# Performance work log

Measured on AMD Instinct MI355X. Metric: run time of the kernel, lower is better.

Reference implementation:

```python
import jax, jax.numpy as jnp
import numpy as np

N = 400000      # simplices (edges of the complexes)
E = 2400000     # nnz of each Laplacian
F_IN = 32
H = 64
KAPPA = 3
G = 512         # graphs in batch
N_OUT = 8
EPS = 1e-5


def spmm(edge_index, edge_values, x, n):
    # y[i] = sum_e val_e * x[j],  i = edge_index[0], j = edge_index[1]
    msg = edge_values[:, None] * x[edge_index[1]]
    return jax.ops.segment_sum(msg, edge_index[0], num_segments=n)


def sc_layer(x, li, lv, ui, uv, Wl, bl, Wu, bu, Wh, bh):
    # SCNN layer: z_low + z_up + z_har (aggr_x fused in)
    n = x.shape[0]
    z = x @ Wh + bh                       # harmonic / identity term
    xl = x
    for k in range(KAPPA):
        xl = spmm(li, lv, xl, n)          # L_low^{k+1} x
        z = z + xl @ Wl[k] + bl[k]
    xu = x
    for k in range(KAPPA):
        xu = spmm(ui, uv, xu, n)          # L_up^{k+1} x
        z = z + xu @ Wu[k] + bu[k]
    return z


def batch_norm(x, gamma, beta):
    mean = jnp.mean(x, axis=0)
    var = jnp.mean((x - mean) ** 2, axis=0)   # biased, as torch BN training
    return (x - mean) * jax.lax.rsqrt(var + EPS) * gamma + beta


def setup_inputs() -> dict:
    key = jax.random.key(0)
    ks = jax.random.split(key, 32)
    s_in = 1.0 / np.sqrt(F_IN)
    s_h = 1.0 / np.sqrt(H)
    inp = {
        "x": jax.random.normal(ks[0], (N, F_IN), jnp.float32),
        "lower_edge_index": jax.random.randint(ks[1], (2, E), 0, N),
        "lower_edge_values": jax.random.normal(ks[2], (E,), jnp.float32),
        "upper_edge_index": jax.random.randint(ks[3], (2, E), 0, N),
        "upper_edge_values": jax.random.normal(ks[4], (E,), jnp.float32),
        "batch_index": jnp.sort(jax.random.randint(ks[5], (N,), 0, G)),
        # layer 0 (F_IN -> H)
        "l0_Wl": jax.random.normal(ks[6], (KAPPA, F_IN, H), jnp.float32) * s_in,
        "l0_bl": jnp.zeros((KAPPA, H), jnp.float32),
        "l0_Wu": jax.random.normal(ks[7], (KAPPA, F_IN, H), jnp.float32) * s_in,
        "l0_bu": jnp.zeros((KAPPA, H), jnp.float32),
        "l0_Wh": jax.random.normal(ks[8], (F_IN, H), jnp.float32) * s_in,
        "l0_bh": jnp.zeros((H,), jnp.float32),
        # layer 1 (H -> H)
        "l1_Wl": jax.random.normal(ks[9], (KAPPA, H, H), jnp.float32) * s_h,
        "l1_bl": jnp.zeros((KAPPA, H), jnp.float32),
        "l1_Wu": jax.random.normal(ks[10], (KAPPA, H, H), jnp.float32) * s_h,
        "l1_bu": jnp.zeros((KAPPA, H), jnp.float32),
        "l1_Wh": jax.random.normal(ks[11], (H, H), jnp.float32) * s_h,
        "l1_bh": jnp.zeros((H,), jnp.float32),
        # batch norms
        "bn0_g": jnp.ones((H,), jnp.float32),
        "bn0_b": jnp.zeros((H,), jnp.float32),
        "bn1_g": jnp.ones((H,), jnp.float32),
        "bn1_b": jnp.zeros((H,), jnp.float32),
        # output MLP [2H, H, N_OUT]
        "mlp_W1": jax.random.normal(ks[12], (2 * H, H), jnp.float32) / np.sqrt(2 * H),
        "mlp_b1": jnp.zeros((H,), jnp.float32),
        "mlp_W2": jax.random.normal(ks[13], (H, N_OUT), jnp.float32) * s_h,
        "mlp_b2": jnp.zeros((N_OUT,), jnp.float32),
    }
    return inp


def reference(x, lower_edge_values, upper_edge_values,
              l0_Wl, l0_bl, l0_Wu, l0_bu, l0_Wh, l0_bh,
              l1_Wl, l1_bl, l1_Wu, l1_bu, l1_Wh, l1_bh,
              bn0_g, bn0_b, bn1_g, bn1_b,
              mlp_W1, mlp_b1, mlp_W2, mlp_b2,
              lower_edge_index, upper_edge_index, batch_index):
    li, ui, bi = lower_edge_index, upper_edge_index, batch_index
    lv, uv = lower_edge_values, upper_edge_values

    h = sc_layer(x, li, lv, ui, uv, l0_Wl, l0_bl, l0_Wu, l0_bu, l0_Wh, l0_bh)
    h = jax.nn.elu(batch_norm(h, bn0_g, bn0_b))
    h = sc_layer(h, li, lv, ui, uv, l1_Wl, l1_bl, l1_Wu, l1_bu, l1_Wh, l1_bh)
    h = jax.nn.elu(batch_norm(h, bn1_g, bn1_b))

    # global max pool + global mean pool per graph
    gmax = jax.ops.segment_max(h, bi, num_segments=G)
    gsum = jax.ops.segment_sum(h, bi, num_segments=G)
    cnt = jax.ops.segment_sum(jnp.ones((h.shape[0],), h.dtype), bi, num_segments=G)
    gmean = gsum / jnp.maximum(cnt, 1.0)[:, None]
    g = jax.nn.elu(jnp.concatenate([gmax, gmean], axis=1))  # [G, 2H]

    # MLP [2H -> H -> N_OUT]
    g = jax.nn.relu(g @ mlp_W1 + mlp_b1)
    return g @ mlp_W2 + mlp_b2
```

## Files before the change

### kernel.cpp

```cpp
#include <hip/hip_runtime.h>
#include <hip/hip_bf16.h>
#include <math.h>

#define N_SIMP 400000
#define E_NNZ  2400000
#define FIN    32
#define HDIM   64
#define KAPPA  3
#define G_NUM  512
#define NOUT   8
#define BN_EPS 1e-5

#define NDIG_HALF 391
#define NDIG      782
#define P1_EDGES  16384
#define P1_BLOCKS 293
#define P1_T      1024
#define P1_EPT    16
#define P2_CAP    7168
#define P2_T      512
#define P2_ITERS  14

typedef __hip_bfloat16 bf16;
typedef _Float16 f16;
typedef short s8v __attribute__((ext_vector_type(8)));
typedef ushort u8v __attribute__((ext_vector_type(8)));
typedef _Float16 h8v __attribute__((ext_vector_type(8)));
typedef float f4v __attribute__((ext_vector_type(4)));

__device__ __forceinline__ float elu_f(float x) {
    return x > 0.f ? x : expm1f(x);
}
__device__ __forceinline__ float bf2f(ushort u) {
    return __uint_as_float(((unsigned int)u) << 16);
}
__device__ __forceinline__ ushort f2bf(float f) {
    bf16 h = (bf16)f;
    return *(ushort*)&h;
}


__global__ __launch_bounds__(P1_T, 1) void p1_sort_kernel(
        const int* __restrict__ eiL, const float* __restrict__ lv,
        const int* __restrict__ eiU, const float* __restrict__ uv,
        int* __restrict__ ccnt, int* __restrict__ bofsv,
        int2* __restrict__ coarse) {
    __shared__ int2 rec[P1_EDGES];
    __shared__ int h[NDIG];
    __shared__ int hscan[P1_T];
    int t = threadIdx.x;
    for (int j = t; j < NDIG; j += P1_T) h[j] = 0;
    __syncthreads();
    int base_i = blockIdx.x * P1_EDGES;
    int key[P1_EPT], val[P1_EPT], dg[P1_EPT];
#pragma unroll
    for (int k = 0; k < P1_EPT; ++k) {
        int i = base_i + k * P1_T + t;
        int dd = -1;
        if (i < 2 * E_NNZ) {
            int row, col;
            float v;
            if (i < E_NNZ) {
                row = eiL[i]; col = eiL[E_NNZ + i]; v = lv[i];
                dd = row >> 10;
            } else {
                int e = i - E_NNZ;
                row = eiU[e]; col = eiU[E_NNZ + e]; v = uv[e];
                dd = NDIG_HALF + (row >> 10);
            }
            key[k] = ((row & 1023) << 22) | col;
            val[k] = __float_as_int(v);
            atomicAdd(&h[dd], 1);
        }
        dg[k] = dd;
    }
    __syncthreads();
    int cv = (t < NDIG) ? h[t] : 0;
    hscan[t] = cv;
    __syncthreads();
    for (int off = 1; off < P1_T; off <<= 1) {
        int x = (t >= off) ? hscan[t - off] : 0;
        __syncthreads();
        hscan[t] += x;
        __syncthreads();
    }
    if (t < NDIG) {
        int ex = hscan[t] - cv;
        ccnt[blockIdx.x * NDIG + t] = cv;
        bofsv[blockIdx.x * NDIG + t] = ex;
        h[t] = ex;
    }
    __syncthreads();
#pragma unroll
    for (int k = 0; k < P1_EPT; ++k) {
        if (dg[k] >= 0) {
            int pos = atomicAdd(&h[dg[k]], 1);
            rec[pos] = make_int2(key[k], val[k]);
        }
    }
    __syncthreads();
    int2* dst = coarse + (size_t)blockIdx.x * P1_EDGES;
    int nrec = 2 * E_NNZ - base_i;
    if (nrec > P1_EDGES) nrec = P1_EDGES;
    for (int j = t; j < nrec; j += P1_T) dst[j] = rec[j];
}

__global__ void digit_total_kernel(const int* __restrict__ cnt, int* __restrict__ tot) {
    int d = blockIdx.x * 256 + threadIdx.x;
    if (d >= NDIG) return;
    int run = 0;
    for (int b = 0; b < P1_BLOCKS; ++b) run += cnt[b * NDIG + d];
    tot[d] = run;
}

__global__ __launch_bounds__(1024) void scan_base_kernel(int* __restrict__ tot) {
    __shared__ int s[1024];
    int t = threadIdx.x;
    int v = (t < NDIG) ? tot[t] : 0;
    s[t] = v;
    __syncthreads();
    for (int off = 1; off < 1024; off <<= 1) {
        int x = (t >= off) ? s[t - off] : 0;
        __syncthreads();
        s[t] += x;
        __syncthreads();
    }
    if (t < NDIG) tot[t] = s[t] - v;
    if (t == 1023) tot[NDIG] = s[1023];
}


__global__ __launch_bounds__(P2_T) void p2_build_kernel(
        const int2* __restrict__ coarse, const int* __restrict__ ccnt,
        const int* __restrict__ bofsv, const int* __restrict__ basev,
        int* __restrict__ rpL, int* __restrict__ rpU,
        int2* __restrict__ edgeL, int2* __restrict__ edgeU) {
    __shared__ int pk[P2_CAP];
    __shared__ int vl[P2_CAP];
    __shared__ int hist[1024];
    __shared__ int sc[P2_T];
    __shared__ int fo[P1_BLOCKS];
    __shared__ int stot;
    int d = blockIdx.x;
    int t = threadIdx.x;
    int len = 0, ofs = 0;
    if (t < P1_BLOCKS) { len = ccnt[t * NDIG + d]; ofs = bofsv[t * NDIG + d]; }
    sc[t] = len;
    __syncthreads();
    for (int off = 1; off < P2_T; off <<= 1) {
        int x = (t >= off) ? sc[t - off] : 0;
        __syncthreads();
        sc[t] += x;
        __syncthreads();
    }
    if (t < P1_BLOCKS) { fo[t] = sc[t] - len; hist[t] = len; hist[512 + t] = ofs; }
    if (t == P1_BLOCKS - 1) stot = sc[t];
    __syncthreads();
    int sz = stot;
    if (sz > P2_CAP) sz = P2_CAP;
    int wv = t >> 6, lane = t & 63;
    for (int b = wv; b < P1_BLOCKS; b += P2_T / 64) {
        int L = hist[b], O = hist[512 + b], F = fo[b];
        const int2* sp = coarse + (size_t)b * P1_EDGES + O;
        for (int j = lane; j < L; j += 64) {
            int dst2 = F + j;
            if (dst2 < P2_CAP) {
                int2 r = sp[j];
                pk[dst2] = r.x;
                vl[dst2] = r.y;
            }
        }
    }
    __syncthreads();
    hist[t] = 0;
    hist[t + P2_T] = 0;
    __syncthreads();
    int myrank[P2_ITERS];
#pragma unroll
    for (int k = 0; k < P2_ITERS; ++k) {
        int j = k * P2_T + t;
        myrank[k] = (j < sz) ? atomicAdd(&hist[((unsigned)pk[j]) >> 22], 1) : 0;
    }
    __syncthreads();
    int h0 = hist[2 * t], h1 = hist[2 * t + 1];
    sc[t] = h0 + h1;
    __syncthreads();
    for (int off = 1; off < P2_T; off <<= 1) {
        int x = (t >= off) ? sc[t - off] : 0;
        __syncthreads();
        sc[t] += x;
        __syncthreads();
    }
    int pbase = sc[t] - (h0 + h1);
    __syncthreads();
    hist[2 * t] = pbase;
    hist[2 * t + 1] = pbase + h0;
    int which = (d >= NDIG_HALF);
    int lbase = basev[d] - (which ? E_NNZ : 0);
    int rowbase = (which ? d - NDIG_HALF : d) << 10;
    int* rp = which ? rpU : rpL;
    int r0 = rowbase + 2 * t, r1 = r0 + 1;
    if (r0 < N_SIMP) rp[r0] = lbase + pbase;
    if (r1 < N_SIMP) rp[r1] = lbase + pbase + h0;
    __syncthreads();
    int2* eout = which ? edgeU : edgeL;
#pragma unroll
    for (int k = 0; k < P2_ITERS; ++k) {
        int j = k * P2_T + t;
        if (j < sz) {
            unsigned p = (unsigned)pk[j];
            int pos = lbase + hist[p >> 22] + myrank[k];
            eout[pos] = make_int2((int)(p & 0x3FFFFF), vl[j]);
        }
    }
}


__global__ void combine_bias_kernel(const float* __restrict__ bh,
                                    const float* __restrict__ bl,
                                    const float* __restrict__ bu,
                                    float* __restrict__ out) {
    int h = threadIdx.x;
    float acc = bh[h];
    for (int k = 0; k < KAPPA; ++k) acc += bl[k * HDIM + h] + bu[k * HDIM + h];
    out[h] = acc;
}

__global__ void f32_to_bf16_kernel(const float* __restrict__ in, bf16* __restrict__ out) {
    int idx = blockIdx.x * 256 + threadIdx.x;
    float4 v = ((const float4*)in)[idx];
    ushort4 w;
    w.x = f2bf(v.x); w.y = f2bf(v.y); w.z = f2bf(v.z); w.w = f2bf(v.w);
    ((ushort4*)out)[idx] = w;
}

__global__ void wtrans_all_kernel(const float* __restrict__ s0, const float* __restrict__ s1,
                                  const float* __restrict__ s2, const float* __restrict__ s3,
                                  const float* __restrict__ s4, const float* __restrict__ s5,
                                  ushort* __restrict__ wt) {
    int idx = blockIdx.x * 256 + threadIdx.x;
    const float* src; int Ktot, off;
    if (idx < 2048)       { src = s0; Ktot = 32;  off = 0; }
    else if (idx < 6144)  { src = s1; Ktot = 64;  off = 2048; }
    else if (idx < 12288) { src = s2; Ktot = 96;  off = 6144; }
    else if (idx < 18432) { src = s3; Ktot = 96;  off = 12288; }
    else if (idx < 30720) { src = s4; Ktot = 192; off = 18432; }
    else                  { src = s5; Ktot = 192; off = 30720; }
    int rel = idx - off;
    int n = rel / Ktot, kk = rel - n * Ktot;
    wt[idx] = f2bf(src[kk * 64 + n]);
}


__global__ void spmm32_kernel(const int* __restrict__ rp, const int2* __restrict__ edge,
                              const bf16* __restrict__ srcb, int src_stride,
                              bf16* __restrict__ dstb) {
    const ushort* src = (const ushort*)srcb;
    ushort* dst = (ushort*)dstb;
    int tid = threadIdx.x;
    int lane = tid & 63;
    int wv = tid >> 6;
    int grp = lane >> 2;
    int li = lane & 3;
    int row = blockIdx.x * 64 + wv * 16 + grp;
    int s = rp[row];
    int e = (row == N_SIMP - 1) ? E_NNZ : rp[row + 1];
    int deg = e - s;
    float a[8] = {0.f, 0.f, 0.f, 0.f, 0.f, 0.f, 0.f, 0.f};
    if (deg > 0) {
        int2 ed[8];
#pragma unroll
        for (int t = 0; t < 8; ++t) {
            int j = s + t;
            ed[t] = edge[(j < e) ? j : (e - 1)];
        }
        u8v xs[8];
#pragma unroll
        for (int t = 0; t < 8; ++t)
            xs[t] = *(const u8v*)(src + (size_t)ed[t].x * src_stride + li * 8);
#pragma unroll
        for (int t = 0; t < 8; ++t) {
            float v = (t < deg) ? __int_as_float(ed[t].y) : 0.f;
#pragma unroll
            for (int c = 0; c < 8; ++c) a[c] += v * bf2f(xs[t][c]);
        }
        for (int j = s + 8; j < e; j += 4) {
            int2 e2[4];
#pragma unroll
            for (int t = 0; t < 4; ++t) {
                int jj = j + t;
                e2[t] = edge[(jj < e) ? jj : (e - 1)];
            }
            u8v x2[4];
#pragma unroll
            for (int t = 0; t < 4; ++t)
                x2[t] = *(const u8v*)(src + (size_t)e2[t].x * src_stride + li * 8);
#pragma unroll
            for (int t = 0; t < 4; ++t) {
                float v = (j + t < e) ? __int_as_float(e2[t].y) : 0.f;
#pragma unroll
                for (int c = 0; c < 8; ++c) a[c] += v * bf2f(x2[t][c]);
            }
        }
    }
    u8v w;
#pragma unroll
    for (int c = 0; c < 8; ++c) w[c] = f2bf(a[c]);
    *(u8v*)(dst + (size_t)row * 32 + li * 8) = w;
}

__global__ void spmm64_kernel(const int* __restrict__ rp, const int2* __restrict__ edge,
                              const bf16* __restrict__ srcb, bf16* __restrict__ dstb) {
    const ushort* src = (const ushort*)srcb;
    ushort* dst = (ushort*)dstb;
    int tid = threadIdx.x;
    int lane = tid & 63;
    int wv = tid >> 6;
    int grp = lane >> 3;
    int li = lane & 7;
    int row = blockIdx.x * 32 + wv * 8 + grp;
    int s = rp[row];
    int e = (row == N_SIMP - 1) ? E_NNZ : rp[row + 1];
    int deg = e - s;
    float a[8] = {0.f, 0.f, 0.f, 0.f, 0.f, 0.f, 0.f, 0.f};
    if (deg > 0) {
        int2 ed[8];
#pragma unroll
        for (int t = 0; t < 8; ++t) {
            int j = s + t;
            ed[t] = edge[(j < e) ? j : (e - 1)];
        }
        u8v xs[8];
#pragma unroll
        for (int t = 0; t < 8; ++t)
            xs[t] = *(const u8v*)(src + (size_t)ed[t].x * 64 + li * 8);
#pragma unroll
        for (int t = 0; t < 8; ++t) {
            float v = (t < deg) ? __int_as_float(ed[t].y) : 0.f;
#pragma unroll
            for (int c = 0; c < 8; ++c) a[c] += v * bf2f(xs[t][c]);
        }
        for (int j = s + 8; j < e; j += 4) {
            int2 e2[4];
#pragma unroll
            for (int t = 0; t < 4; ++t) {
                int jj = j + t;
                e2[t] = edge[(jj < e) ? jj : (e - 1)];
            }
            u8v x2[4];
#pragma unroll
            for (int t = 0; t < 4; ++t)
                x2[t] = *(const u8v*)(src + (size_t)e2[t].x * 64 + li * 8);
#pragma unroll
            for (int t = 0; t < 4; ++t) {
                float v = (j + t < e) ? __int_as_float(e2[t].y) : 0.f;
#pragma unroll
                for (int c = 0; c < 8; ++c) a[c] += v * bf2f(x2[t][c]);
            }
        }
    }
    u8v w;
#pragma unroll
    for (int c = 0; c < 8; ++c) w[c] = f2bf(a[c]);
    *(u8v*)(dst + (size_t)row * 64 + li * 8) = w;
}


template <int NCH, int NCH1, bool INIT>
__global__ __launch_bounds__(256) void mfma_gemm_kernel(
        const ushort* __restrict__ s0, int st0,
        const ushort* __restrict__ s1, int st1,
        const ushort* __restrict__ s2, int st2,
        const ushort* __restrict__ s3, int st3,
        const ushort* __restrict__ s4, int st4,
        const ushort* __restrict__ s5, int st5,
        const ushort* __restrict__ Wt1, int Kstride1,
        const ushort* __restrict__ Wt2, int Kstride2,
        const float* __restrict__ bias,
        f16* __restrict__ z) {
    int tid = threadIdx.x;
    int wv = tid >> 6, lane = tid & 63;
    int quad = lane >> 4, n = lane & 15;
    int rowbase = blockIdx.x * 64 + wv * 16;
    int arow = rowbase + n;

    f4v acc0 = {0.f, 0.f, 0.f, 0.f};
    f4v acc1 = {0.f, 0.f, 0.f, 0.f};
    f4v acc2 = {0.f, 0.f, 0.f, 0.f};
    f4v acc3 = {0.f, 0.f, 0.f, 0.f};

#pragma unroll
    for (int ch = 0; ch < NCH; ++ch) {
        const ushort* sp = (ch == 0) ? s0 : (ch == 1) ? s1 : (ch == 2) ? s2
                         : (ch == 3) ? s3 : (ch == 4) ? s4 : s5;
        int st = (ch == 0) ? st0 : (ch == 1) ? st1 : (ch == 2) ? st2
               : (ch == 3) ? st3 : (ch == 4) ? st4 : st5;
        const ushort* wb = (ch < NCH1) ? (Wt1 + ch * 32) : (Wt2 + (ch - NCH1) * 32);
        int Ks = (ch < NCH1) ? Kstride1 : Kstride2;
        s8v a = *(const s8v*)(sp + (size_t)arow * st + quad * 8);
        const ushort* wq = wb + quad * 8;
        s8v b0 = *(const s8v*)(wq + (size_t)(0 * 16 + n) * Ks);
        s8v b1 = *(const s8v*)(wq + (size_t)(1 * 16 + n) * Ks);
        s8v b2 = *(const s8v*)(wq + (size_t)(2 * 16 + n) * Ks);
        s8v b3 = *(const s8v*)(wq + (size_t)(3 * 16 + n) * Ks);
        acc0 = __builtin_amdgcn_mfma_f32_16x16x32_bf16(a, b0, acc0, 0, 0, 0);
        acc1 = __builtin_amdgcn_mfma_f32_16x16x32_bf16(a, b1, acc1, 0, 0, 0);
        acc2 = __builtin_amdgcn_mfma_f32_16x16x32_bf16(a, b2, acc2, 0, 0, 0);
        acc3 = __builtin_amdgcn_mfma_f32_16x16x32_bf16(a, b3, acc3, 0, 0, 0);
    }
#pragma unroll
    for (int r = 0; r < 4; ++r) {
        int orow = rowbase + quad * 4 + r;
        f16* zp = z + (size_t)orow * 64 + n;
        if (INIT) {
            zp[0]  = (f16)(bias[n]      + acc0[r]);
            zp[16] = (f16)(bias[16 + n] + acc1[r]);
            zp[32] = (f16)(bias[32 + n] + acc2[r]);
            zp[48] = (f16)(bias[48 + n] + acc3[r]);
        } else {
            zp[0]  = (f16)((float)zp[0]  + acc0[r]);
            zp[16] = (f16)((float)zp[16] + acc1[r]);
            zp[32] = (f16)((float)zp[32] + acc2[r]);
            zp[48] = (f16)((float)zp[48] + acc3[r]);
        }
    }
}


__global__ void bn_stats_kernel(const f16* __restrict__ z, double* __restrict__ stats) {
    __shared__ float ss[256 * 8], qq[256 * 8];
    int tid = threadIdx.x;
    const h8v* z8 = (const h8v*)z;
    const int total8 = N_SIMP * HDIM / 8;
    float fs[8] = {0, 0, 0, 0, 0, 0, 0, 0};
    float fq[8] = {0, 0, 0, 0, 0, 0, 0, 0};
    for (int i = blockIdx.x * 256 + tid; i < total8; i += (int)gridDim.x * 256) {
        h8v v = z8[i];
#pragma unroll
        for (int c = 0; c < 8; ++c) {
            float f = (float)v[c];
            fs[c] += f;
            fq[c] += f * f;
        }
    }
#pragma unroll
    for (int c = 0; c < 8; ++c) { ss[tid * 8 + c] = fs[c]; qq[tid * 8 + c] = fq[c]; }
    __syncthreads();
    if (tid < 64) {
        int sel = tid >> 3, slot = tid & 7;
        double a = 0.0, b = 0.0;
#pragma unroll 8
        for (int k = 0; k < 32; ++k) {
            int t = sel + (k << 3);
            a += (double)ss[t * 8 + slot];
            b += (double)qq[t * 8 + slot];
        }
        atomicAdd(&stats[tid], a);
        atomicAdd(&stats[64 + tid], b);
    }
}

__global__ void bn_elu_bf16_kernel(const f16* __restrict__ z, const double* __restrict__ stats,
                                   const float* __restrict__ gamma, const float* __restrict__ beta,
                                   bf16* __restrict__ out) {
    __shared__ float scale_s[64], shift_s[64];
    int tid = threadIdx.x;
    if (tid < 64) {
        double mean = stats[tid] / (double)N_SIMP;
        double var = stats[64 + tid] / (double)N_SIMP - mean * mean;
        double sc = (double)gamma[tid] / sqrt(var + BN_EPS);
        scale_s[tid] = (float)sc;
        shift_s[tid] = (float)((double)beta[tid] - mean * sc);
    }
    __syncthreads();
    const h8v* z8 = (const h8v*)z;
    u8v* o8 = (u8v*)out;
    const int total8 = N_SIMP * HDIM / 8;
    int hb = (tid & 7) * 8;
    for (int i = blockIdx.x * 256 + tid; i < total8; i += (int)gridDim.x * 256) {
        h8v v = z8[i];
        u8v w;
#pragma unroll
        for (int c = 0; c < 8; ++c)
            w[c] = f2bf(elu_f((float)v[c] * scale_s[hb + c] + shift_s[hb + c]));
        o8[i] = w;
    }
}

__global__ void bn_elu_f16_kernel(f16* __restrict__ z, const double* __restrict__ stats,
                                  const float* __restrict__ gamma, const float* __restrict__ beta) {
    __shared__ float scale_s[64], shift_s[64];
    int tid = threadIdx.x;
    if (tid < 64) {
        double mean = stats[tid] / (double)N_SIMP;
        double var = stats[64 + tid] / (double)N_SIMP - mean * mean;
        double sc = (double)gamma[tid] / sqrt(var + BN_EPS);
        scale_s[tid] = (float)sc;
        shift_s[tid] = (float)((double)beta[tid] - mean * sc);
    }
    __syncthreads();
    h8v* z8 = (h8v*)z;
    const int total8 = N_SIMP * HDIM / 8;
    int hb = (tid & 7) * 8;
    for (int i = blockIdx.x * 256 + tid; i < total8; i += (int)gridDim.x * 256) {
        h8v v = z8[i];
        h8v w;
#pragma unroll
        for (int c = 0; c < 8; ++c)
            w[c] = (f16)elu_f((float)v[c] * scale_s[hb + c] + shift_s[hb + c]);
        z8[i] = w;
    }
}

__global__ void pool_kernel(const f16* __restrict__ hbuf, const int* __restrict__ bidx,
                            float* __restrict__ gbuf) {
    __shared__ float smax[256], ssum[256];
    int g = blockIdx.x;
    int tid = threadIdx.x;
    int lo = 0, hi = N_SIMP;
    while (lo < hi) { int mid = (lo + hi) >> 1; if (bidx[mid] < g) lo = mid + 1; else hi = mid; }
    int start = lo;
    hi = N_SIMP;
    while (lo < hi) { int mid = (lo + hi) >> 1; if (bidx[mid] < g + 1) lo = mid + 1; else hi = mid; }
    int end = lo;
    int h = tid & 63, rep = tid >> 6;
    float mx = -INFINITY, sm = 0.f;
    for (int i = start + rep; i < end; i += 4) {
        float v = (float)hbuf[(size_t)i * HDIM + h];
        mx = fmaxf(mx, v);
        sm += v;
    }
    smax[tid] = mx; ssum[tid] = sm;
    __syncthreads();
    if (tid < 64) {
        float m = fmaxf(fmaxf(smax[tid], smax[tid + 64]), fmaxf(smax[tid + 128], smax[tid + 192]));
        float s = ssum[tid] + ssum[tid + 64] + ssum[tid + 128] + ssum[tid + 192];
        int cnt = end - start;
        float mean = s / fmaxf((float)cnt, 1.f);
        gbuf[g * 128 + tid] = elu_f(m);
        gbuf[g * 128 + 64 + tid] = elu_f(mean);
    }
}

__global__ void mlp_kernel(const float* __restrict__ gbuf, const float* __restrict__ W1,
                           const float* __restrict__ b1, const float* __restrict__ W2,
                           const float* __restrict__ b2, float* __restrict__ out) {
    __shared__ float gs[128];
    __shared__ float hs[64];
    int g = blockIdx.x, tid = threadIdx.x;
    gs[tid] = gbuf[g * 128 + tid];
    gs[64 + tid] = gbuf[g * 128 + 64 + tid];
    __syncthreads();
    float acc = b1[tid];
#pragma unroll
    for (int k = 0; k < 128; ++k) acc += gs[k] * W1[k * 64 + tid];
    hs[tid] = fmaxf(acc, 0.f);
    __syncthreads();
    if (tid < 8) {
        float o = b2[tid];
#pragma unroll
        for (int k = 0; k < 64; ++k) o += hs[k] * W2[k * 8 + tid];
        out[g * 8 + tid] = o;
    }
}


extern "C" void kernel_launch(void* const* d_in, const int* in_sizes, int n_in,
                              void* d_out, int out_size, void* d_ws, size_t ws_size,
                              hipStream_t stream) {
    const float* x     = (const float*)d_in[0];
    const int*   li    = (const int*)d_in[1];
    const float* lv    = (const float*)d_in[2];
    const int*   ui    = (const int*)d_in[3];
    const float* uv    = (const float*)d_in[4];
    const int*   bidx  = (const int*)d_in[5];
    const float* l0_Wl = (const float*)d_in[6];
    const float* l0_bl = (const float*)d_in[7];
    const float* l0_Wu = (const float*)d_in[8];
    const float* l0_bu = (const float*)d_in[9];
    const float* l0_Wh = (const float*)d_in[10];
    const float* l0_bh = (const float*)d_in[11];
    const float* l1_Wl = (const float*)d_in[12];
    const float* l1_bl = (const float*)d_in[13];
    const float* l1_Wu = (const float*)d_in[14];
    const float* l1_bu = (const float*)d_in[15];
    const float* l1_Wh = (const float*)d_in[16];
    const float* l1_bh = (const float*)d_in[17];
    const float* bn0_g = (const float*)d_in[18];
    const float* bn0_b = (const float*)d_in[19];
    const float* bn1_g = (const float*)d_in[20];
    const float* bn1_b = (const float*)d_in[21];
    const float* mW1   = (const float*)d_in[22];
    const float* mb1   = (const float*)d_in[23];
    const float* mW2   = (const float*)d_in[24];
    const float* mb2   = (const float*)d_in[25];
    float* out = (float*)d_out;

    char* base = (char*)d_ws;
    f16*   z     = (f16*)base;
    bf16*  h0bf  = (bf16*)(base + 51200000ull);
    bf16*  g1    = (bf16*)(base + 102400000ull);
    bf16*  g2    = (bf16*)(base + 153600000ull);
    int2*  edgeL = (int2*)(base + 204800000ull);
    int2*  edgeU = (int2*)(base + 224000000ull);
    int*   rpL   = (int*)(base + 243200000ull);
    int*   rpU   = (int*)(base + 244800032ull);
    double* stats = (double*)(base + 246404160ull);
    float* cbias  = (float*)(base + 246405184ull);
    float* gbuf   = (float*)(base + 246405440ull);
    ushort* wt    = (ushort*)(base + 246667584ull);

    int2* coarse = (int2*)base;
    int*  basev  = (int*)(base + 38500000ull);
    int*  ccnt   = (int*)(base + 51200000ull);
    int*  bofsv  = (int*)(base + 52200000ull);

    bf16* xbf  = g1;
    bf16* cAL  = g1 + (size_t)N_SIMP * 32;
    bf16* cBL  = g2;
    bf16* cCL  = g2 + (size_t)N_SIMP * 32;
    bf16* cAU  = h0bf;
    bf16* cBU  = h0bf + (size_t)N_SIMP * 32;
    bf16* cCU  = g1;

    ushort* wt_l0h = wt;
    ushort* wt_l1h = wt + 2048;
    ushort* wt_l0l = wt + 6144;
    ushort* wt_l0u = wt + 12288;
    ushort* wt_l1l = wt + 18432;
    ushort* wt_l1u = wt + 30720;

    const int SP32_BLOCKS = N_SIMP / 64;
    const int SP64_BLOCKS = N_SIMP / 32;
    const int MF_BLOCKS   = N_SIMP / 64;

    wtrans_all_kernel<<<168, 256, 0, stream>>>(l0_Wh, l1_Wh, l0_Wl, l0_Wu, l1_Wl, l1_Wu, wt);
    f32_to_bf16_kernel<<<N_SIMP * 32 / 4 / 256, 256, 0, stream>>>(x, xbf);

    p1_sort_kernel<<<P1_BLOCKS, P1_T, 0, stream>>>(li, lv, ui, uv, ccnt, bofsv, coarse);
    digit_total_kernel<<<(NDIG + 255) / 256, 256, 0, stream>>>(ccnt, basev);
    scan_base_kernel<<<1, 1024, 0, stream>>>(basev);
    p2_build_kernel<<<NDIG, P2_T, 0, stream>>>(coarse, ccnt, bofsv, basev,
                                               rpL, rpU, edgeL, edgeU);

    const ushort* xbfu = (const ushort*)xbf;
    const ushort* h0u  = (const ushort*)h0bf;
    const ushort* g1u  = (const ushort*)g1;
    const ushort* g2u  = (const ushort*)g2;

    combine_bias_kernel<<<1, 64, 0, stream>>>(l0_bh, l0_bl, l0_bu, cbias);
    mfma_gemm_kernel<1, 1, true><<<MF_BLOCKS, 256, 0, stream>>>(
        xbfu, 32, nullptr, 0, nullptr, 0, nullptr, 0, nullptr, 0, nullptr, 0,
        wt_l0h, 32, wt_l0h, 32, cbias, z);

    spmm32_kernel<<<SP32_BLOCKS, 256, 0, stream>>>(rpL, edgeL, xbf, 32, cAL);
    spmm32_kernel<<<SP32_BLOCKS, 256, 0, stream>>>(rpL, edgeL, cAL, 32, cBL);
    spmm32_kernel<<<SP32_BLOCKS, 256, 0, stream>>>(rpL, edgeL, cBL, 32, cCL);
    spmm32_kernel<<<SP32_BLOCKS, 256, 0, stream>>>(rpU, edgeU, xbf, 32, cAU);
    spmm32_kernel<<<SP32_BLOCKS, 256, 0, stream>>>(rpU, edgeU, cAU, 32, cBU);
    spmm32_kernel<<<SP32_BLOCKS, 256, 0, stream>>>(rpU, edgeU, cBU, 32, cCU);
    mfma_gemm_kernel<6, 3, false><<<MF_BLOCKS, 256, 0, stream>>>(
        (const ushort*)cAL, 32, (const ushort*)cBL, 32, (const ushort*)cCL, 32,
        (const ushort*)cAU, 32, (const ushort*)cBU, 32, (const ushort*)cCU, 32,
        wt_l0l, 96, wt_l0u, 96, nullptr, z);

    (void)hipMemsetAsync(stats, 0, 128 * sizeof(double), stream);
    bn_stats_kernel<<<1024, 256, 0, stream>>>(z, stats);
    bn_elu_bf16_kernel<<<1024, 256, 0, stream>>>(z, stats, bn0_g, bn0_b, h0bf);

    combine_bias_kernel<<<1, 64, 0, stream>>>(l1_bh, l1_bl, l1_bu, cbias);
    mfma_gemm_kernel<2, 2, true><<<MF_BLOCKS, 256, 0, stream>>>(
        h0u, 64, h0u + 32, 64, nullptr, 0, nullptr, 0, nullptr, 0, nullptr, 0,
        wt_l1h, 64, wt_l1h, 64, cbias, z);

    spmm64_kernel<<<SP64_BLOCKS, 256, 0, stream>>>(rpL, edgeL, h0bf, g1);
    spmm64_kernel<<<SP64_BLOCKS, 256, 0, stream>>>(rpL, edgeL, g1, g2);
    mfma_gemm_kernel<4, 4, false><<<MF_BLOCKS, 256, 0, stream>>>(
        g1u, 64, g1u + 32, 64, g2u, 64, g2u + 32, 64, nullptr, 0, nullptr, 0,
        wt_l1l, 192, wt_l1l, 192, nullptr, z);
    spmm64_kernel<<<SP64_BLOCKS, 256, 0, stream>>>(rpL, edgeL, g2, g1);
    spmm64_kernel<<<SP64_BLOCKS, 256, 0, stream>>>(rpU, edgeU, h0bf, g2);
    mfma_gemm_kernel<4, 2, false><<<MF_BLOCKS, 256, 0, stream>>>(
        g1u, 64, g1u + 32, 64, g2u, 64, g2u + 32, 64, nullptr, 0, nullptr, 0,
        wt_l1l + 128, 192, wt_l1u, 192, nullptr, z);
    spmm64_kernel<<<SP64_BLOCKS, 256, 0, stream>>>(rpU, edgeU, g2, g1);
    spmm64_kernel<<<SP64_BLOCKS, 256, 0, stream>>>(rpU, edgeU, g1, g2);
    mfma_gemm_kernel<4, 4, false><<<MF_BLOCKS, 256, 0, stream>>>(
        g1u, 64, g1u + 32, 64, g2u, 64, g2u + 32, 64, nullptr, 0, nullptr, 0,
        wt_l1u + 64, 192, wt_l1u + 64, 192, nullptr, z);

    (void)hipMemsetAsync(stats, 0, 128 * sizeof(double), stream);
    bn_stats_kernel<<<1024, 256, 0, stream>>>(z, stats);
    bn_elu_f16_kernel<<<1024, 256, 0, stream>>>(z, stats, bn1_g, bn1_b);

    pool_kernel<<<G_NUM, 256, 0, stream>>>(z, bidx, gbuf);
    mlp_kernel<<<G_NUM, 64, 0, stream>>>(gbuf, mW1, mb1, mW2, mb2, out);
}
```

Baseline: 1.391 ms.

## Fuse final BN+ELU into pooling and merge layer-1 harmonic GEMM

```diff
diff --git a/kernel.cpp b/kernel.cpp
--- a/kernel.cpp
+++ b/kernel.cpp
@@ -487,9 +487,12 @@
     }
 }
 
-__global__ void bn_elu_f16_kernel(f16* __restrict__ z, const double* __restrict__ stats,
-                                  const float* __restrict__ gamma, const float* __restrict__ beta) {
+__global__ void pool_bn_kernel(const f16* __restrict__ zbuf, const int* __restrict__ bidx,
+                               const double* __restrict__ stats,
+                               const float* __restrict__ gamma, const float* __restrict__ beta,
+                               float* __restrict__ gbuf) {
     __shared__ float scale_s[64], shift_s[64];
+    __shared__ float pmax[256 * 8], psum[256 * 8];
     int tid = threadIdx.x;
     if (tid < 64) {
         double mean = stats[tid] / (double)N_SIMP;
@@ -499,42 +502,43 @@
         shift_s[tid] = (float)((double)beta[tid] - mean * sc);
     }
     __syncthreads();
-    h8v* z8 = (h8v*)z;
-    const int total8 = N_SIMP * HDIM / 8;
-    int hb = (tid & 7) * 8;
-    for (int i = blockIdx.x * 256 + tid; i < total8; i += (int)gridDim.x * 256) {
-        h8v v = z8[i];
-        h8v w;
-#pragma unroll
-        for (int c = 0; c < 8; ++c)
-            w[c] = (f16)elu_f((float)v[c] * scale_s[hb + c] + shift_s[hb + c]);
-        z8[i] = w;
-    }
-}
-
-__global__ void pool_kernel(const f16* __restrict__ hbuf, const int* __restrict__ bidx,
-                            float* __restrict__ gbuf) {
-    __shared__ float smax[256], ssum[256];
     int g = blockIdx.x;
-    int tid = threadIdx.x;
     int lo = 0, hi = N_SIMP;
     while (lo < hi) { int mid = (lo + hi) >> 1; if (bidx[mid] < g) lo = mid + 1; else hi = mid; }
     int start = lo;
     hi = N_SIMP;
     while (lo < hi) { int mid = (lo + hi) >> 1; if (bidx[mid] < g + 1) lo = mid + 1; else hi = mid; }
     int end = lo;
-    int h = tid & 63, rep = tid >> 6;
-    float mx = -INFINITY, sm = 0.f;
-    for (int i = start + rep; i < end; i += 4) {
-        float v = (float)hbuf[(size_t)i * HDIM + h];
-        mx = fmaxf(mx, v);
-        sm += v;
-    }
-    smax[tid] = mx; ssum[tid] = sm;
+    int li = tid & 7;
+    int rr = tid >> 3;
+    const h8v* z8 = (const h8v*)zbuf;
+    float mx[8], sm[8];
+#pragma unroll
+    for (int c = 0; c < 8; ++c) { mx[c] = -INFINITY; sm[c] = 0.f; }
+    float sc8[8], sh8[8];
+#pragma unroll
+    for (int c = 0; c < 8; ++c) { sc8[c] = scale_s[li * 8 + c]; sh8[c] = shift_s[li * 8 + c]; }
+    for (int i = start + rr; i < end; i += 32) {
+        h8v v = z8[(size_t)i * 8 + li];
+#pragma unroll
+        for (int c = 0; c < 8; ++c) {
+            float y = elu_f((float)v[c] * sc8[c] + sh8[c]);
+            mx[c] = fmaxf(mx[c], y);
+            sm[c] += y;
+        }
+    }
+#pragma unroll
+    for (int c = 0; c < 8; ++c) { pmax[tid * 8 + c] = mx[c]; psum[tid * 8 + c] = sm[c]; }
     __syncthreads();
     if (tid < 64) {
-        float m = fmaxf(fmaxf(smax[tid], smax[tid + 64]), fmaxf(smax[tid + 128], smax[tid + 192]));
-        float s = ssum[tid] + ssum[tid + 64] + ssum[tid + 128] + ssum[tid + 192];
+        int sel = tid >> 3, slot = tid & 7;
+        float m = -INFINITY, s = 0.f;
+#pragma unroll 8
+        for (int k = 0; k < 32; ++k) {
+            int t = k * 8 + sel;
+            m = fmaxf(m, pmax[t * 8 + slot]);
+            s += psum[t * 8 + slot];
+        }
         int cnt = end - start;
         float mean = s / fmaxf((float)cnt, 1.f);
         gbuf[g * 128 + tid] = elu_f(m);
@@ -669,15 +673,12 @@
     bn_elu_bf16_kernel<<<1024, 256, 0, stream>>>(z, stats, bn0_g, bn0_b, h0bf);
 
     combine_bias_kernel<<<1, 64, 0, stream>>>(l1_bh, l1_bl, l1_bu, cbias);
-    mfma_gemm_kernel<2, 2, true><<<MF_BLOCKS, 256, 0, stream>>>(
-        h0u, 64, h0u + 32, 64, nullptr, 0, nullptr, 0, nullptr, 0, nullptr, 0,
-        wt_l1h, 64, wt_l1h, 64, cbias, z);
 
     spmm64_kernel<<<SP64_BLOCKS, 256, 0, stream>>>(rpL, edgeL, h0bf, g1);
     spmm64_kernel<<<SP64_BLOCKS, 256, 0, stream>>>(rpL, edgeL, g1, g2);
-    mfma_gemm_kernel<4, 4, false><<<MF_BLOCKS, 256, 0, stream>>>(
-        g1u, 64, g1u + 32, 64, g2u, 64, g2u + 32, 64, nullptr, 0, nullptr, 0,
-        wt_l1l, 192, wt_l1l, 192, nullptr, z);
+    mfma_gemm_kernel<6, 2, true><<<MF_BLOCKS, 256, 0, stream>>>(
+        h0u, 64, h0u + 32, 64, g1u, 64, g1u + 32, 64, g2u, 64, g2u + 32, 64,
+        wt_l1h, 64, wt_l1l, 192, cbias, z);
     spmm64_kernel<<<SP64_BLOCKS, 256, 0, stream>>>(rpL, edgeL, g2, g1);
     spmm64_kernel<<<SP64_BLOCKS, 256, 0, stream>>>(rpU, edgeU, h0bf, g2);
     mfma_gemm_kernel<4, 2, false><<<MF_BLOCKS, 256, 0, stream>>>(
@@ -691,8 +692,7 @@
 
     (void)hipMemsetAsync(stats, 0, 128 * sizeof(double), stream);
     bn_stats_kernel<<<1024, 256, 0, stream>>>(z, stats);
-    bn_elu_f16_kernel<<<1024, 256, 0, stream>>>(z, stats, bn1_g, bn1_b);
-
-    pool_kernel<<<G_NUM, 256, 0, stream>>>(z, bidx, gbuf);
+
+    pool_bn_kernel<<<G_NUM, 256, 0, stream>>>(z, bidx, stats, bn1_g, bn1_b, gbuf);
     mlp_kernel<<<G_NUM, 64, 0, stream>>>(gbuf, mW1, mb1, mW2, mb2, out);
 }
```

Result: faster. 1.324 ms (-4.8%).
